# Performance work log

Hardware: AMD Instinct MI355X
Metric: run time of the kernel (lower is better)

## Reference

```python
import jax, jax.numpy as jnp
import numpy as np

H_IMG, W_IMG = 128, 128            # image size (init arg)
FX, FY = 120.0, 120.0              # camera intrinsics (read from COLMAP cfg in original __init__)
CX, CY = 64.0, 64.0
N_GAUSS = 65536
N_POSES = 2
EPS = 1e-8


def quat2mat(q):
    q = q / jnp.linalg.norm(q)
    w, x, y, z = q[0], q[1], q[2], q[3]
    return jnp.stack([
        jnp.stack([1 - 2 * (y * y + z * z), 2 * (x * y - z * w), 2 * (x * z + y * w)]),
        jnp.stack([2 * (x * y + z * w), 1 - 2 * (x * x + z * z), 2 * (y * z - x * w)]),
        jnp.stack([2 * (x * z - y * w), 2 * (y * z + x * w), 1 - 2 * (x * x + y * y)]),
    ])


def _forward(positions, colors, opacities, scales, qvec, tvec, tile_hw, chunk_gauss):
    HW = H_IMG * W_IMG
    step = tile_hw * tile_hw          # pixels per tile (contiguous in flat row-major order)
    n_tiles = HW // step
    N = positions.shape[0]
    n_chunks = N // chunk_gauss
    xs = jnp.arange(W_IMG, dtype=jnp.float32)
    ys = jnp.arange(H_IMG, dtype=jnp.float32)
    yy, xx = jnp.meshgrid(ys, xs, indexing='ij')
    px = xx.reshape(-1)               # [HW] pixel x coords
    py = yy.reshape(-1)               # [HW] pixel y coords
    var_c = (scales[:, 0] ** 2).reshape(n_chunks, chunk_gauss)
    op_c = opacities[:, 0].reshape(n_chunks, chunk_gauss)
    col_c = colors.reshape(n_chunks, chunk_gauss, 3)

    def render_pose(q, t):
        R = quat2mat(q)
        cam = positions @ R.T + t                                 # [N,3] camera-space points
        uv = jnp.stack([cam[:, 0] / cam[:, 2] * FX + CX,
                        cam[:, 1] / cam[:, 2] * FY + CY], 1)      # [N,2] pixel-space centers
        uv_c = uv.reshape(n_chunks, chunk_gauss, 2)

        def body(acc, chunk):
            uvg, vg, og, cg = chunk                               # [C,2],[C],[C],[C,3]
            d2 = (px[None, :] - uvg[:, 0:1]) ** 2 + (py[None, :] - uvg[:, 1:2]) ** 2  # [C,HW]
            w = og[:, None] * jnp.exp(-0.5 * d2 / vg[:, None])    # [C,HW] splat weights
            return (acc[0] + w.T @ cg, acc[1] + w.sum(0)), None

        init = (jnp.zeros((HW, 3), jnp.float32), jnp.zeros((HW,), jnp.float32))
        (num, den), _ = jax.lax.scan(body, init, (uv_c, var_c, op_c, col_c))
        # original adds 1e-8 to the denominator once per gaussian chunk
        img = num / (den + n_chunks * EPS)[:, None]               # [HW,3] normalized blend
        # per tile of `step` flat pixels: [step,3].T -> [3,tile_hw,tile_hw]
        return img.reshape(n_tiles, step, 3).transpose(0, 2, 1).reshape(n_tiles, 3, tile_hw, tile_hw)

    out = jax.vmap(render_pose)(qvec, tvec)                       # [B, n_tiles, 3, th, th]
    return out.reshape(-1, 3, tile_hw, tile_hw)


def setup_inputs() -> dict:
    key = jax.random.key(0)
    ks = jax.random.split(key, 6)
    positions = jax.random.normal(ks[0], (N_GAUSS, 3), jnp.float32) * 1.5
    positions = positions.at[:, 2].set(jnp.abs(positions[:, 2]) + 4.0)  # keep z>0 (in front of camera)
    colors = jax.random.uniform(ks[1], (N_GAUSS, 3), jnp.float32)
    opacities = jax.random.uniform(ks[2], (N_GAUSS, 1), jnp.float32)
    scales = jax.random.uniform(ks[3], (N_GAUSS, 1), jnp.float32) * 2.0 + 1.0  # var strictly > 0
    qvec = jax.random.normal(ks[4], (N_POSES, 4), jnp.float32)
    tvec = jax.random.normal(ks[5], (N_POSES, 3), jnp.float32) * 0.1
    return {"positions": positions, "colors": colors, "opacities": opacities,
            "scales": scales, "qvec": qvec, "tvec": tvec,
            "tile_hw": 32, "chunk_gauss": 4096}


def reference(positions, colors, opacities, scales, qvec, tvec, tile_hw, chunk_gauss):
    return _forward(positions, colors, opacities, scales, qvec, tvec, tile_hw, chunk_gauss)
```

## Files before the change

### kernel.cpp

```cpp
#include <hip/hip_runtime.h>


#define H_IMG 128
#define W_IMG 128
#define FX_C 120.0f
#define FY_C 120.0f
#define CX_C 64.0f
#define CY_C 64.0f
#define NG 65536
#define SLAB 1024
#define KSPLIT 64
#define KC 64
#define NCHUNK 16
#define APAD 72
#define NEG_HALF_LOG2E -0.72134752044448170f
#define EPS_TOT 1.6e-7f

#if __has_builtin(__builtin_amdgcn_exp2f)
#define EXP2(x) __builtin_amdgcn_exp2f(x)
#else
#define EXP2(x) exp2f(x)
#endif

typedef __attribute__((ext_vector_type(8))) short short8;
typedef __attribute__((ext_vector_type(4))) float f32x4;

__device__ __forceinline__ unsigned bfpk2(float a, float b) {
    return __builtin_amdgcn_perm(__float_as_uint(b) + 0x8000u,
                                 __float_as_uint(a) + 0x8000u,
                                 0x07060302u);
}

__global__ void zero_accum_kernel(float* __restrict__ p) {
    p[blockIdx.x * 256 + threadIdx.x] = 0.0f;
}

template <bool STORE>
__global__ __launch_bounds__(1024) void render_kernel(
    const float* __restrict__ gpos, const float* __restrict__ gcol,
    const float* __restrict__ gopa, const float* __restrict__ gscl,
    const float* __restrict__ qvec, const float* __restrict__ tvec,
    float* __restrict__ accum,
    float* __restrict__ pbuf)
{
    __shared__ ushort A_lds[64][APAD];
    __shared__ ushort B_lds[512][APAD];
    __shared__ float u_s[SLAB], v_s[SLAB], ke_s[SLAB];
    __shared__ float wc_s[4][SLAB];

    const int split = blockIdx.x;
    const int ph    = blockIdx.y;
    const int pose  = ph >> 1;
    const int half  = ph & 1;
    const int tid   = threadIdx.x;

    float q0 = qvec[pose*4+0], q1 = qvec[pose*4+1], q2 = qvec[pose*4+2], q3 = qvec[pose*4+3];
    float rn = rsqrtf(q0*q0 + q1*q1 + q2*q2 + q3*q3);
    float qw = q0*rn, qx = q1*rn, qy = q2*rn, qz = q3*rn;
    float r00 = 1.0f-2.0f*(qy*qy+qz*qz), r01 = 2.0f*(qx*qy-qz*qw), r02 = 2.0f*(qx*qz+qy*qw);
    float r10 = 2.0f*(qx*qy+qz*qw), r11 = 1.0f-2.0f*(qx*qx+qz*qz), r12 = 2.0f*(qy*qz-qx*qw);
    float r20 = 2.0f*(qx*qz-qy*qw), r21 = 2.0f*(qy*qz+qx*qw), r22 = 1.0f-2.0f*(qx*qx+qy*qy);
    float tx = tvec[pose*3+0], ty = tvec[pose*3+1], tz = tvec[pose*3+2];

    {
        int g = split*SLAB + tid;
        float p0 = gpos[g*3+0], p1 = gpos[g*3+1], p2 = gpos[g*3+2];
        float cxm = r00*p0 + r01*p1 + r02*p2 + tx;
        float cym = r10*p0 + r11*p1 + r12*p2 + ty;
        float czm = r20*p0 + r21*p1 + r22*p2 + tz;
        float iz  = 1.0f / czm;
        u_s[tid] = cxm*iz*FX_C + CX_C;
        v_s[tid] = cym*iz*FY_C + CY_C;
        float s  = gscl[g];
        ke_s[tid] = NEG_HALF_LOG2E / (s*s);
        float og = gopa[g];
        wc_s[0][tid] = og * gcol[g*3+0];
        wc_s[1][tid] = og * gcol[g*3+1];
        wc_s[2][tid] = og * gcol[g*3+2];
        wc_s[3][tid] = og;
    }
    __syncthreads();

    const int rowA = tid >> 4;
    const int qg   = (tid & 15) << 2;
    const float cjA = (float)(half*64 + rowA);
    const int row_x = tid >> 3;
    const int oct   = (tid & 7) << 3;
    const float cjB = (float)row_x;

    const int lane = tid & 63;
    const int wave = tid >> 6;
    const int wy   = wave >> 3;
    const int wn   = wave & 7;

    f32x4 acc0[4] = {};
    f32x4 acc1[4] = {};

    for (int ch = 0; ch < NCHUNK; ++ch) {
        {
            const int gb = (ch << 6) + qg;
            const float4 kv = *(const float4*)&ke_s[gb];
            const float4 vv = *(const float4*)&v_s[gb];
            float d, f0, f1, f2, f3;
            d = cjA - vv.x; f0 = EXP2(kv.x*d*d);
            d = cjA - vv.y; f1 = EXP2(kv.y*d*d);
            d = cjA - vv.z; f2 = EXP2(kv.z*d*d);
            d = cjA - vv.w; f3 = EXP2(kv.w*d*d);
            uint2 pk;
            pk.x = bfpk2(f0, f1); pk.y = bfpk2(f2, f3);
            *(uint2*)&A_lds[rowA][qg] = pk;
        }
        {
            const int gb = (ch << 6) + oct;
            const float4 ka = *(const float4*)&ke_s[gb];
            const float4 kb = *(const float4*)&ke_s[gb+4];
            const float4 ua = *(const float4*)&u_s[gb];
            const float4 ub = *(const float4*)&u_s[gb+4];
            float d, x0,x1,x2,x3,x4,x5,x6,x7;
            d = cjB - ua.x; x0 = EXP2(ka.x*d*d);
            d = cjB - ua.y; x1 = EXP2(ka.y*d*d);
            d = cjB - ua.z; x2 = EXP2(ka.z*d*d);
            d = cjB - ua.w; x3 = EXP2(ka.w*d*d);
            d = cjB - ub.x; x4 = EXP2(kb.x*d*d);
            d = cjB - ub.y; x5 = EXP2(kb.y*d*d);
            d = cjB - ub.z; x6 = EXP2(kb.z*d*d);
            d = cjB - ub.w; x7 = EXP2(kb.w*d*d);
            #pragma unroll
            for (int c = 0; c < 4; ++c) {
                const float4 wa = *(const float4*)&wc_s[c][gb];
                const float4 wb = *(const float4*)&wc_s[c][gb+4];
                uint4 pk;
                pk.x = bfpk2(x0*wa.x, x1*wa.y);
                pk.y = bfpk2(x2*wa.z, x3*wa.w);
                pk.z = bfpk2(x4*wb.x, x5*wb.y);
                pk.w = bfpk2(x6*wb.z, x7*wb.w);
                *(uint4*)&B_lds[(c << 7) + row_x][oct] = pk;
            }
        }
        __syncthreads();
        {
            const int kq = (lane >> 4) << 3;
            #pragma unroll
            for (int ks = 0; ks < 2; ++ks) {
                const int ko = ks*32 + kq;
                short8 a0 = *(const short8*)&A_lds[wy*32      + (lane & 15)][ko];
                short8 a1 = *(const short8*)&A_lds[wy*32 + 16 + (lane & 15)][ko];
                #pragma unroll
                for (int ni = 0; ni < 4; ++ni) {
                    short8 bf = *(const short8*)&B_lds[wn*64 + ni*16 + (lane & 15)][ko];
                    acc0[ni] = __builtin_amdgcn_mfma_f32_16x16x32_bf16(a0, bf, acc0[ni], 0, 0, 0);
                    acc1[ni] = __builtin_amdgcn_mfma_f32_16x16x32_bf16(a1, bf, acc1[ni], 0, 0, 0);
                }
            }
        }
        __syncthreads();
    }

    const int m_base = wy*32 + ((lane >> 4) << 2);
    const int n_base = wn*64 + (lane & 15);
    if (STORE) {
        float* bp = pbuf + ((size_t)(ph*KSPLIT + split) * 64 + m_base) * 512 + n_base;
        #pragma unroll
        for (int ni = 0; ni < 4; ++ni) {
            #pragma unroll
            for (int r = 0; r < 4; ++r) {
                bp[r*512        + ni*16] = acc0[ni][r];
                bp[(16 + r)*512 + ni*16] = acc1[ni][r];
            }
        }
    } else {
        float* bp = accum + ((size_t)(pose*H_IMG + half*64 + m_base) * 512 + n_base);
        #pragma unroll
        for (int ni = 0; ni < 4; ++ni) {
            #pragma unroll
            for (int r = 0; r < 4; ++r) {
                atomicAdd(bp + r*512        + ni*16, acc0[ni][r]);
                atomicAdd(bp + (16 + r)*512 + ni*16, acc1[ni][r]);
            }
        }
    }
}

__global__ __launch_bounds__(1024) void reduce_norm_kernel(
    const float* __restrict__ pbuf, float* __restrict__ out)
{
    __shared__ float red[2][512];
    const int b  = blockIdx.x;
    const int p  = b >> 7;
    const int y  = b & 127;
    const int ph = p*2 + (y >> 6);
    const int yl = y & 63;
    const int t  = threadIdx.x;
    const int sg = t >> 9;
    const int n  = t & 511;

    const float* base = pbuf + ((size_t)(ph*KSPLIT + sg*32) * 64 + yl) * 512 + n;
    float s = 0.0f;
    #pragma unroll 8
    for (int i = 0; i < 32; ++i) s += base[(size_t)i * 32768];
    red[sg][n] = s;
    __syncthreads();

    if (t < 384) {
        const int c = t >> 7, x = t & 127;
        float den = red[0][384 + x] + red[1][384 + x];
        float num = red[0][t]       + red[1][t];
        float inv = 1.0f / (den + EPS_TOT);
        int tt = y >> 3;
        int q  = ((y & 7) << 7) + x;
        out[(size_t)((p*16 + tt)*3 + c) * 1024 + q] = num * inv;
    }
}

__global__ void normalize_kernel(const float* __restrict__ acc, float* __restrict__ out) {
    int idx = blockIdx.x * 256 + threadIdx.x;
    int x = idx & 127;
    int y = (idx >> 7) & 127;
    int p = idx >> 14;
    const float* base = acc + (size_t)(p*128 + y) * 512;
    float inv = 1.0f / (base[384 + x] + EPS_TOT);
    int t = y >> 3;
    int q = ((y & 7) << 7) + x;
    float* ob = out + (size_t)((p*16 + t)*3) * 1024 + q;
    ob[0]    = base[x]       * inv;
    ob[1024] = base[128 + x] * inv;
    ob[2048] = base[256 + x] * inv;
}

extern "C" void kernel_launch(void* const* d_in, const int* in_sizes, int n_in,
                              void* d_out, int out_size, void* d_ws, size_t ws_size,
                              hipStream_t stream) {
    const float* gpos = (const float*)d_in[0];
    const float* gcol = (const float*)d_in[1];
    const float* gopa = (const float*)d_in[2];
    const float* gscl = (const float*)d_in[3];
    const float* qv   = (const float*)d_in[4];
    const float* tv   = (const float*)d_in[5];
    float* out = (float*)d_out;

    const size_t need = (size_t)4 * KSPLIT * 64 * 512 * sizeof(float);

    if (ws_size >= need) {
        float* pbuf = (float*)d_ws;
        render_kernel<true><<<dim3(KSPLIT, 4), dim3(1024), 0, stream>>>(
            gpos, gcol, gopa, gscl, qv, tv, nullptr, pbuf);
        reduce_norm_kernel<<<dim3(256), dim3(1024), 0, stream>>>(pbuf, out);
    } else {
        float* acc = (float*)d_ws;
        zero_accum_kernel<<<dim3(512), dim3(256), 0, stream>>>(acc);
        render_kernel<false><<<dim3(KSPLIT, 4), dim3(1024), 0, stream>>>(
            gpos, gcol, gopa, gscl, qv, tv, acc, nullptr);
        normalize_kernel<<<dim3(128), dim3(256), 0, stream>>>(acc, out);
    }
}
```

Before: 117.6 us.

## Split MFMA K across wave halves with 64x64 per-wave tiles and LDS reduction

Each wave now computes a full 64x64 output tile over half of the 64-wide K chunk, instead of a 32x64 tile over the whole chunk. This gives more register reuse of A and B fragments per MFMA. The two K halves are then summed through LDS scratch before the store. Operand construction is also reassigned: half the threads build B (4 x rows each) and half build A (2 y rows each), which rebalances exp work. The cost is more accumulator registers (64 floats), possibly lower occupancy, and an extra reduction phase with barriers.

Measured after the change: 114.9 us. 2.3% less time.

```diff
diff --git a/kernel.cpp b/kernel.cpp
--- a/kernel.cpp
+++ b/kernel.cpp
@@ -10,7 +10,6 @@
 #define NG 65536
 #define SLAB 1024
 #define KSPLIT 64
-#define KC 64
 #define NCHUNK 16
 #define APAD 72
 #define NEG_HALF_LOG2E -0.72134752044448170f
@@ -81,102 +80,123 @@
     }
     __syncthreads();
 
-    const int rowA = tid >> 4;
-    const int qg   = (tid & 15) << 2;
-    const float cjA = (float)(half*64 + rowA);
-    const int row_x = tid >> 3;
-    const int oct   = (tid & 7) << 3;
-    const float cjB = (float)row_x;
-
     const int lane = tid & 63;
     const int wave = tid >> 6;
-    const int wy   = wave >> 3;
-    const int wn   = wave & 7;
-
-    f32x4 acc0[4] = {};
-    f32x4 acc1[4] = {};
+    const int kset = wave >> 3;
+    const int wn8  = wave & 7;
+
+    const bool isB = (tid < 512);
+    const int st   = isB ? tid : (tid - 512);
+    const int g4   = (st & 15) << 2;
+    const int grp  = st >> 4;
+
+    const int arow = lane & 15;
+    const int kcol = kset*32 + ((lane >> 4) << 3);
+
+    f32x4 acc[4][4] = {};
 
     for (int ch = 0; ch < NCHUNK; ++ch) {
-        {
-            const int gb = (ch << 6) + qg;
+        const int gb = (ch << 6) + g4;
+        if (isB) {
+            const float4 kv = *(const float4*)&ke_s[gb];
+            const float4 uv = *(const float4*)&u_s[gb];
+            float e[4][4];
+            #pragma unroll
+            for (int xi = 0; xi < 4; ++xi) {
+                const float xf = (float)(grp*4 + xi);
+                float d;
+                d = xf - uv.x; e[xi][0] = EXP2(kv.x*d*d);
+                d = xf - uv.y; e[xi][1] = EXP2(kv.y*d*d);
+                d = xf - uv.z; e[xi][2] = EXP2(kv.z*d*d);
+                d = xf - uv.w; e[xi][3] = EXP2(kv.w*d*d);
+            }
+            #pragma unroll
+            for (int c = 0; c < 4; ++c) {
+                const float4 wv = *(const float4*)&wc_s[c][gb];
+                #pragma unroll
+                for (int xi = 0; xi < 4; ++xi) {
+                    uint2 pk;
+                    pk.x = bfpk2(e[xi][0]*wv.x, e[xi][1]*wv.y);
+                    pk.y = bfpk2(e[xi][2]*wv.z, e[xi][3]*wv.w);
+                    *(uint2*)&B_lds[(c << 7) + grp*4 + xi][g4] = pk;
+                }
+            }
+        } else {
             const float4 kv = *(const float4*)&ke_s[gb];
             const float4 vv = *(const float4*)&v_s[gb];
-            float d, f0, f1, f2, f3;
-            d = cjA - vv.x; f0 = EXP2(kv.x*d*d);
-            d = cjA - vv.y; f1 = EXP2(kv.y*d*d);
-            d = cjA - vv.z; f2 = EXP2(kv.z*d*d);
-            d = cjA - vv.w; f3 = EXP2(kv.w*d*d);
-            uint2 pk;
-            pk.x = bfpk2(f0, f1); pk.y = bfpk2(f2, f3);
-            *(uint2*)&A_lds[rowA][qg] = pk;
-        }
+            #pragma unroll
+            for (int yi = 0; yi < 2; ++yi) {
+                const float yf = (float)(half*64 + grp*2 + yi);
+                float d, f0, f1, f2, f3;
+                d = yf - vv.x; f0 = EXP2(kv.x*d*d);
+                d = yf - vv.y; f1 = EXP2(kv.y*d*d);
+                d = yf - vv.z; f2 = EXP2(kv.z*d*d);
+                d = yf - vv.w; f3 = EXP2(kv.w*d*d);
+                uint2 pk;
+                pk.x = bfpk2(f0, f1); pk.y = bfpk2(f2, f3);
+                *(uint2*)&A_lds[grp*2 + yi][g4] = pk;
+            }
+        }
+        __syncthreads();
         {
-            const int gb = (ch << 6) + oct;
-            const float4 ka = *(const float4*)&ke_s[gb];
-            const float4 kb = *(const float4*)&ke_s[gb+4];
-            const float4 ua = *(const float4*)&u_s[gb];
-            const float4 ub = *(const float4*)&u_s[gb+4];
-            float d, x0,x1,x2,x3,x4,x5,x6,x7;
-            d = cjB - ua.x; x0 = EXP2(ka.x*d*d);
-            d = cjB - ua.y; x1 = EXP2(ka.y*d*d);
-            d = cjB - ua.z; x2 = EXP2(ka.z*d*d);
-            d = cjB - ua.w; x3 = EXP2(ka.w*d*d);
-            d = cjB - ub.x; x4 = EXP2(kb.x*d*d);
-            d = cjB - ub.y; x5 = EXP2(kb.y*d*d);
-            d = cjB - ub.z; x6 = EXP2(kb.z*d*d);
-            d = cjB - ub.w; x7 = EXP2(kb.w*d*d);
-            #pragma unroll
-            for (int c = 0; c < 4; ++c) {
-                const float4 wa = *(const float4*)&wc_s[c][gb];
-                const float4 wb = *(const float4*)&wc_s[c][gb+4];
-                uint4 pk;
-                pk.x = bfpk2(x0*wa.x, x1*wa.y);
-                pk.y = bfpk2(x2*wa.z, x3*wa.w);
-                pk.z = bfpk2(x4*wb.x, x5*wb.y);
-                pk.w = bfpk2(x6*wb.z, x7*wb.w);
-                *(uint4*)&B_lds[(c << 7) + row_x][oct] = pk;
-            }
-        }
-        __syncthreads();
-        {
-            const int kq = (lane >> 4) << 3;
-            #pragma unroll
-            for (int ks = 0; ks < 2; ++ks) {
-                const int ko = ks*32 + kq;
-                short8 a0 = *(const short8*)&A_lds[wy*32      + (lane & 15)][ko];
-                short8 a1 = *(const short8*)&A_lds[wy*32 + 16 + (lane & 15)][ko];
-                #pragma unroll
-                for (int ni = 0; ni < 4; ++ni) {
-                    short8 bf = *(const short8*)&B_lds[wn*64 + ni*16 + (lane & 15)][ko];
-                    acc0[ni] = __builtin_amdgcn_mfma_f32_16x16x32_bf16(a0, bf, acc0[ni], 0, 0, 0);
-                    acc1[ni] = __builtin_amdgcn_mfma_f32_16x16x32_bf16(a1, bf, acc1[ni], 0, 0, 0);
-                }
-            }
-        }
-        __syncthreads();
-    }
-
-    const int m_base = wy*32 + ((lane >> 4) << 2);
-    const int n_base = wn*64 + (lane & 15);
-    if (STORE) {
-        float* bp = pbuf + ((size_t)(ph*KSPLIT + split) * 64 + m_base) * 512 + n_base;
-        #pragma unroll
-        for (int ni = 0; ni < 4; ++ni) {
-            #pragma unroll
-            for (int r = 0; r < 4; ++r) {
-                bp[r*512        + ni*16] = acc0[ni][r];
-                bp[(16 + r)*512 + ni*16] = acc1[ni][r];
-            }
-        }
-    } else {
-        float* bp = accum + ((size_t)(pose*H_IMG + half*64 + m_base) * 512 + n_base);
-        #pragma unroll
-        for (int ni = 0; ni < 4; ++ni) {
-            #pragma unroll
-            for (int r = 0; r < 4; ++r) {
-                atomicAdd(bp + r*512        + ni*16, acc0[ni][r]);
-                atomicAdd(bp + (16 + r)*512 + ni*16, acc1[ni][r]);
-            }
+            short8 a[4], b[4];
+            #pragma unroll
+            for (int mt = 0; mt < 4; ++mt)
+                a[mt] = *(const short8*)&A_lds[mt*16 + arow][kcol];
+            #pragma unroll
+            for (int nt = 0; nt < 4; ++nt)
+                b[nt] = *(const short8*)&B_lds[wn8*64 + nt*16 + arow][kcol];
+            #pragma unroll
+            for (int mt = 0; mt < 4; ++mt)
+                #pragma unroll
+                for (int nt = 0; nt < 4; ++nt)
+                    acc[mt][nt] = __builtin_amdgcn_mfma_f32_16x16x32_bf16(a[mt], b[nt], acc[mt][nt], 0, 0, 0);
+        }
+        __syncthreads();
+    }
+
+    f32x4* scr = (f32x4*)&B_lds[0][0];
+    #pragma unroll
+    for (int r = 0; r < 2; ++r) {
+        if (kset == 1) {
+            #pragma unroll
+            for (int m2 = 0; m2 < 2; ++m2)
+                #pragma unroll
+                for (int nt = 0; nt < 4; ++nt)
+                    scr[(((wn8*2 + m2)*4 + nt) << 6) + lane] = acc[r*2 + m2][nt];
+        }
+        __syncthreads();
+        if (kset == 0) {
+            #pragma unroll
+            for (int m2 = 0; m2 < 2; ++m2)
+                #pragma unroll
+                for (int nt = 0; nt < 4; ++nt)
+                    acc[r*2 + m2][nt] += scr[(((wn8*2 + m2)*4 + nt) << 6) + lane];
+        }
+        __syncthreads();
+    }
+
+    if (kset == 0) {
+        const int m0 = (lane >> 4) << 2;
+        const int n0 = wn8*64 + (lane & 15);
+        if (STORE) {
+            float* bp = pbuf + ((size_t)(ph*KSPLIT + split) * 64) * 512 + n0;
+            #pragma unroll
+            for (int mt = 0; mt < 4; ++mt)
+                #pragma unroll
+                for (int nt = 0; nt < 4; ++nt)
+                    #pragma unroll
+                    for (int r = 0; r < 4; ++r)
+                        bp[(size_t)(mt*16 + m0 + r)*512 + nt*16] = acc[mt][nt][r];
+        } else {
+            float* bp = accum + ((size_t)(pose*H_IMG + half*64) * 512) + n0;
+            #pragma unroll
+            for (int mt = 0; mt < 4; ++mt)
+                #pragma unroll
+                for (int nt = 0; nt < 4; ++nt)
+                    #pragma unroll
+                    for (int r = 0; r < 4; ++r)
+                        atomicAdd(bp + (size_t)(mt*16 + m0 + r)*512 + nt*16, acc[mt][nt][r]);
         }
     }
 }
```
